# Performance work log

Measured on AMD Instinct MI355X. Metric: run time of the kernel, lower is better.

The kernel has to match this reference:

```python
import jax, jax.numpy as jnp
import numpy as np

NUM_EXPERTS = 256
TOP_K = 8
N_GROUP = 8
TOPK_GROUP = 4
ROUTED_SCALING_FACTOR = 2.5


def setup_inputs() -> dict:
    key = jax.random.key(0)
    k1, k2, k3 = jax.random.split(key, 3)
    B, H, E = 16384, 7168, NUM_EXPERTS
    hidden_states = jax.random.normal(k1, (B, H), dtype=jnp.float32)
    weight = jax.random.normal(k2, (E, H), dtype=jnp.float32) * 0.02
    e_score_correction_bias = jax.random.normal(k3, (E,), dtype=jnp.float32) * 0.01
    return {
        "hidden_states": hidden_states,
        "weight": weight,
        "e_score_correction_bias": e_score_correction_bias,
    }


def reference(hidden_states, weight, e_score_correction_bias):
    B = hidden_states.shape[0]
    experts_per_group = NUM_EXPERTS // N_GROUP
    # router logits: [B, E] (small skinny GEMM)
    router_logits = jnp.einsum("bh,eh->be", hidden_states.astype(jnp.float32), weight.astype(jnp.float32))
    # torch casts to f64 for sigmoid then back; f32 sigmoid is numerically equivalent here
    scores = jax.nn.sigmoid(router_logits).astype(hidden_states.dtype)
    scores_for_choice = scores + e_score_correction_bias[None, :]
    # per-group score = sum of top-2 expert scores in the group
    grp = scores_for_choice.reshape(B, N_GROUP, experts_per_group)
    top2_vals, _ = jax.lax.top_k(grp, 2)          # [B, G, 2]
    group_scores = top2_vals.sum(axis=-1)          # [B, G]
    # pick topk_group groups, build group mask via scatter
    _, group_idx = jax.lax.top_k(group_scores, TOPK_GROUP)  # [B, topk_group]
    group_mask = jnp.zeros((B, N_GROUP), dtype=scores_for_choice.dtype)
    group_mask = group_mask.at[jnp.arange(B)[:, None], group_idx].set(1.0)
    # expand group mask to experts and mask scores
    score_mask = jnp.broadcast_to(group_mask[:, :, None], (B, N_GROUP, experts_per_group)).reshape(B, -1)
    masked_scores = jnp.where(score_mask > 0, scores_for_choice, 0.0)
    # final expert top-k on masked (bias-corrected) scores
    _, topk_indices = jax.lax.top_k(masked_scores, TOP_K)   # [B, top_k]
    # weights gathered from the UN-biased sigmoid scores, then normalize + scale
    topk_weights = jnp.take_along_axis(scores, topk_indices, axis=1)
    topk_weights = topk_weights / topk_weights.sum(axis=-1, keepdims=True)
    topk_weights = topk_weights * ROUTED_SCALING_FACTOR
    return topk_indices, topk_weights
```

## Files before the change

### kernel.cpp

```cpp
#include <hip/hip_runtime.h>
#include <math.h>

#define B_ROWS 16384
#define H_DIM 7168
#define N_EXP 256
#define KT 32
#define MT 64
#define ET 128

using v4d = __attribute__((ext_vector_type(4))) double;

__global__ __launch_bounds__(256, 2)
void router_gemm(const float* __restrict__ hs, const float* __restrict__ w,
                 float* __restrict__ scores) {
    __shared__ float AfU[2304];
    __shared__ float WfU[4608];
    __shared__ int okSh;

    const int t = threadIdx.x;
    const int lane = t & 63;
    const int wv = t >> 6;
    const int fm = lane & 15;
    const int kg = lane >> 4;
    const int tx = t & 15;
    const int ty = t >> 4;
    const int row8 = t >> 3;
    const int kq8 = t & 7;

    const int mBase = blockIdx.x * MT;
    const int eBase = blockIdx.y * ET;
    const float* hsp = hs + (size_t)mBase * H_DIM;
    const float* wp  = w  + (size_t)eBase * H_DIM;

    bool ok = true;
#pragma unroll 1
    for (int p = 0; p < 3; ++p) {
        for (int i = t; i < 64 * 36; i += 256) {
            int m = i / 36, kk = i % 36;
            int k = (kk & 7) * 4 + (kk >> 3);
            AfU[i] = (p == 0) ? (float)(4 * m + k + 1)
                   : (p == 2) ? (float)(k + 1) : 1.0f;
        }
        for (int i = t; i < 128 * 36; i += 256) {
            int e = i / 36, kk = i % 36;
            int k = (kk & 7) * 4 + (kk >> 3);
            WfU[i] = (p == 1) ? (float)(4 * e + k + 1)
                   : (p == 2) ? (float)(k + 1) : 1.0f;
        }
        __syncthreads();
        double a = (double)AfU[fm * 36 + 8 * kg];
        double b = (double)WfU[fm * 36 + 8 * kg];
        v4d z = {0.0, 0.0, 0.0, 0.0};
        v4d pr = __builtin_amdgcn_mfma_f64_16x16x4f64(a, b, z, 0, 0, 0);
#pragma unroll
        for (int r = 0; r < 4; ++r) {
            double ev = (p == 0) ? (double)(16 * (4 * kg + r) + 10)
                      : (p == 1) ? (double)(16 * fm + 10) : 30.0;
            ok = ok && (pr[r] == ev);
        }
        __syncthreads();
    }
    if (t == 0) okSh = 1;
    __syncthreads();
    if (!ok) okSh = 0;
    __syncthreads();
    const bool useMfma = (okSh != 0);

    union AccU { double v[4][8]; v4d m[4][2]; } acc;
#pragma unroll
    for (int r = 0; r < 4; ++r)
#pragma unroll
        for (int c = 0; c < 8; ++c) acc.v[r][c] = 0.0;

    float haf[2][4], waf[4][4];
#pragma unroll
    for (int i = 0; i < 2; ++i)
        *(float4*)&haf[i][0] = *(const float4*)(hsp + (size_t)(i * 32 + row8) * H_DIM + 4 * kq8);
#pragma unroll
    for (int i = 0; i < 4; ++i)
        *(float4*)&waf[i][0] = *(const float4*)(wp + (size_t)(i * 32 + row8) * H_DIM + 4 * kq8);

    const int NCHUNK = H_DIM / KT;
    for (int ch = 0; ch < NCHUNK; ++ch) {
        if (useMfma) {
#pragma unroll
            for (int i = 0; i < 2; ++i)
#pragma unroll
                for (int j = 0; j < 4; ++j)
                    AfU[(i * 32 + row8) * 36 + 8 * j + kq8] = haf[i][j];
#pragma unroll
            for (int i = 0; i < 4; ++i)
#pragma unroll
                for (int j = 0; j < 4; ++j)
                    WfU[(i * 32 + row8) * 36 + 8 * j + kq8] = waf[i][j];
        } else {
#pragma unroll
            for (int i = 0; i < 2; ++i)
#pragma unroll
                for (int j = 0; j < 4; ++j)
                    AfU[(4 * kq8 + j) * 68 + i * 32 + row8] = haf[i][j];
#pragma unroll
            for (int i = 0; i < 4; ++i)
#pragma unroll
                for (int j = 0; j < 4; ++j)
                    WfU[(4 * kq8 + j) * 132 + i * 32 + row8] = waf[i][j];
        }
        __syncthreads();
        if (ch + 1 < NCHUNK) {
            const float* hp2 = hsp + (size_t)(ch + 1) * KT;
            const float* wp2 = wp  + (size_t)(ch + 1) * KT;
#pragma unroll
            for (int i = 0; i < 2; ++i)
                *(float4*)&haf[i][0] = *(const float4*)(hp2 + (size_t)(i * 32 + row8) * H_DIM + 4 * kq8);
#pragma unroll
            for (int i = 0; i < 4; ++i)
                *(float4*)&waf[i][0] = *(const float4*)(wp2 + (size_t)(i * 32 + row8) * H_DIM + 4 * kq8);
        }
        if (useMfma) {
            float afr[4][8], bfr[2][8];
#pragma unroll
            for (int rs = 0; rs < 4; ++rs) {
                const int base = (rs * 16 + fm) * 36 + 8 * kg;
                *(float4*)&afr[rs][0] = *(float4*)&AfU[base];
                *(float4*)&afr[rs][4] = *(float4*)&AfU[base + 4];
            }
#pragma unroll
            for (int cs = 0; cs < 2; ++cs) {
                const int base = (wv * 32 + cs * 16 + fm) * 36 + 8 * kg;
                *(float4*)&bfr[cs][0] = *(float4*)&WfU[base];
                *(float4*)&bfr[cs][4] = *(float4*)&WfU[base + 4];
            }
#pragma unroll
            for (int q = 0; q < 8; ++q) {
                double aq0 = (double)afr[0][q], aq1 = (double)afr[1][q];
                double aq2 = (double)afr[2][q], aq3 = (double)afr[3][q];
                double bq0 = (double)bfr[0][q], bq1 = (double)bfr[1][q];
                acc.m[0][0] = __builtin_amdgcn_mfma_f64_16x16x4f64(aq0, bq0, acc.m[0][0], 0, 0, 0);
                acc.m[0][1] = __builtin_amdgcn_mfma_f64_16x16x4f64(aq0, bq1, acc.m[0][1], 0, 0, 0);
                acc.m[1][0] = __builtin_amdgcn_mfma_f64_16x16x4f64(aq1, bq0, acc.m[1][0], 0, 0, 0);
                acc.m[1][1] = __builtin_amdgcn_mfma_f64_16x16x4f64(aq1, bq1, acc.m[1][1], 0, 0, 0);
                acc.m[2][0] = __builtin_amdgcn_mfma_f64_16x16x4f64(aq2, bq0, acc.m[2][0], 0, 0, 0);
                acc.m[2][1] = __builtin_amdgcn_mfma_f64_16x16x4f64(aq2, bq1, acc.m[2][1], 0, 0, 0);
                acc.m[3][0] = __builtin_amdgcn_mfma_f64_16x16x4f64(aq3, bq0, acc.m[3][0], 0, 0, 0);
                acc.m[3][1] = __builtin_amdgcn_mfma_f64_16x16x4f64(aq3, bq1, acc.m[3][1], 0, 0, 0);
            }
        } else {
#pragma unroll
            for (int k = 0; k < KT; ++k) {
                float4 af  = *(float4*)&AfU[k * 68 + ty * 4];
                float4 bfa = *(float4*)&WfU[k * 132 + tx * 4];
                float4 bfb = *(float4*)&WfU[k * 132 + 64 + tx * 4];
                double a_[4] = {(double)af.x, (double)af.y, (double)af.z, (double)af.w};
                double b_[8] = {(double)bfa.x, (double)bfa.y, (double)bfa.z, (double)bfa.w,
                                (double)bfb.x, (double)bfb.y, (double)bfb.z, (double)bfb.w};
#pragma unroll
                for (int r = 0; r < 4; ++r)
#pragma unroll
                    for (int c = 0; c < 8; ++c)
                        acc.v[r][c] = fma(a_[r], b_[c], acc.v[r][c]);
            }
        }
        __syncthreads();
    }

    if (useMfma) {
#pragma unroll
        for (int rs = 0; rs < 4; ++rs)
#pragma unroll
            for (int cs = 0; cs < 2; ++cs)
#pragma unroll
                for (int r = 0; r < 4; ++r) {
                    const int rr = mBase + rs * 16 + 4 * kg + r;
                    const int cc = eBase + wv * 32 + cs * 16 + fm;
                    double s = 1.0 / (1.0 + exp(-acc.m[rs][cs][r]));
                    scores[(size_t)rr * N_EXP + cc] = (float)s;
                }
    } else {
#pragma unroll
        for (int r = 0; r < 4; ++r) {
            const int rr = mBase + ty * 4 + r;
            float* dst = scores + (size_t)rr * N_EXP + eBase;
            float4 o0, o1;
            o0.x = (float)(1.0 / (1.0 + exp(-acc.v[r][0])));
            o0.y = (float)(1.0 / (1.0 + exp(-acc.v[r][1])));
            o0.z = (float)(1.0 / (1.0 + exp(-acc.v[r][2])));
            o0.w = (float)(1.0 / (1.0 + exp(-acc.v[r][3])));
            o1.x = (float)(1.0 / (1.0 + exp(-acc.v[r][4])));
            o1.y = (float)(1.0 / (1.0 + exp(-acc.v[r][5])));
            o1.z = (float)(1.0 / (1.0 + exp(-acc.v[r][6])));
            o1.w = (float)(1.0 / (1.0 + exp(-acc.v[r][7])));
            *(float4*)(dst + tx * 4) = o0;
            *(float4*)(dst + 64 + tx * 4) = o1;
        }
    }
}

__global__ __launch_bounds__(256)
void router_topk_kernel(const float* __restrict__ scores, const float* __restrict__ bias,
                        float* __restrict__ out) {
    const int lane = threadIdx.x & 63;
    const int row = (blockIdx.x * blockDim.x + threadIdx.x) >> 6;

    float4 s4 = *(const float4*)(scores + (size_t)row * N_EXP + lane * 4);
    float4 b4 = *(const float4*)(bias + lane * 4);
    float sc[4]  = {s4.x, s4.y, s4.z, s4.w};
    float sfc[4] = {sc[0] + b4.x, sc[1] + b4.y, sc[2] + b4.z, sc[3] + b4.w};

    float m1 = -1e30f, m2 = -1e30f;
#pragma unroll
    for (int i = 0; i < 4; ++i) {
        float v = sfc[i];
        if (v > m1) { m2 = m1; m1 = v; }
        else if (v > m2) m2 = v;
    }
#pragma unroll
    for (int off = 1; off <= 4; off <<= 1) {
        float o1 = __shfl_xor(m1, off);
        float o2 = __shfl_xor(m2, off);
        float n1 = fmaxf(m1, o1);
        float n2 = fmaxf(fminf(m1, o1), fmaxf(m2, o2));
        m1 = n1; m2 = n2;
    }
    float gs = m1 + m2;
    int g = lane >> 3;
    int rank = 0;
#pragma unroll
    for (int j = 0; j < 8; ++j) {
        float gj = __shfl(gs, j * 8);
        rank += (gj > gs || (gj == gs && j < g)) ? 1 : 0;
    }
    bool sel = rank < 4;
    float mv[4];
#pragma unroll
    for (int i = 0; i < 4; ++i) mv[i] = sel ? sfc[i] : 0.0f;

    float wsum = 0.f;
    float myIdxF = 0.f, myW = 0.f;
    for (int it = 0; it < 8; ++it) {
        float bv = mv[0]; int bi = 0;
#pragma unroll
        for (int i = 1; i < 4; ++i)
            if (mv[i] > bv) { bv = mv[i]; bi = i; }
        int bidx = lane * 4 + bi;
        float bsc = sc[bi];
#pragma unroll
        for (int off = 1; off <= 32; off <<= 1) {
            float ov = __shfl_xor(bv, off);
            int   oi = __shfl_xor(bidx, off);
            float os = __shfl_xor(bsc, off);
            if (ov > bv || (ov == bv && oi < bidx)) { bv = ov; bidx = oi; bsc = os; }
        }
        wsum += bsc;
        if (lane == it) { myIdxF = (float)bidx; myW = bsc; }
        if ((bidx >> 2) == lane) mv[bidx & 3] = -1e30f;
    }
    if (lane < 8) {
        out[(size_t)row * 8 + lane] = myIdxF;
        out[(size_t)B_ROWS * 8 + (size_t)row * 8 + lane] = myW * (2.5f / wsum);
    }
}

extern "C" void kernel_launch(void* const* d_in, const int* in_sizes, int n_in,
                              void* d_out, int out_size, void* d_ws, size_t ws_size,
                              hipStream_t stream) {
    const float* hs   = (const float*)d_in[0];
    const float* w    = (const float*)d_in[1];
    const float* bias = (const float*)d_in[2];
    float* out = (float*)d_out;
    float* scores = (float*)d_ws;

    dim3 g1(B_ROWS / MT, N_EXP / ET);
    router_gemm<<<g1, 256, 0, stream>>>(hs, w, scores);
    router_topk_kernel<<<B_ROWS / 4, 256, 0, stream>>>(scores, bias, out);
}
```

Measured before the change: 1.986 ms.

## Store MFMA operands as doubles in LDS and probe output layout at runtime

The MFMA path now converts hs and weight tiles to double when writing them to shared memory, with a padded stride of 33, instead of storing floats and converting after each LDS read. This moves the float-to-double conversion from the inner MFMA loop to the staging step, which runs once per element. The startup self-test no longer fills LDS in three passes; it issues a few register-only MFMAs and derives the output row and column mapping from their results, and the store step uses that mapping. In exchange the kernel moves twice as many LDS bytes per chunk as scalar double reads rather than float4 reads, and the larger LDS footprint may reduce occupancy.

Result: faster. 1.589 ms (-20.0%).

```diff
diff --git a/kernel.cpp b/kernel.cpp
--- a/kernel.cpp
+++ b/kernel.cpp
@@ -13,9 +13,12 @@
 __global__ __launch_bounds__(256, 2)
 void router_gemm(const float* __restrict__ hs, const float* __restrict__ w,
                  float* __restrict__ scores) {
-    __shared__ float AfU[2304];
-    __shared__ float WfU[4608];
+    __shared__ double LdsD[64 * 33 + 128 * 33];
     __shared__ int okSh;
+    double* Ad = LdsD;
+    double* Wd = LdsD + 64 * 33;
+    float* Af = (float*)LdsD;
+    float* Wf = ((float*)LdsD) + 2304;
 
     const int t = threadIdx.x;
     const int lane = t & 63;
@@ -32,33 +35,28 @@
     const float* hsp = hs + (size_t)mBase * H_DIM;
     const float* wp  = w  + (size_t)eBase * H_DIM;
 
+    v4d z = {0.0, 0.0, 0.0, 0.0};
+    v4d d1 = __builtin_amdgcn_mfma_f64_16x16x4f64((double)(fm + 1), 1.0, z, 0, 0, 0);
+    v4d d2 = __builtin_amdgcn_mfma_f64_16x16x4f64(1.0, (double)(fm + 1), z, 0, 0, 0);
+    v4d d3 = __builtin_amdgcn_mfma_f64_16x16x4f64((double)(4 * fm + kg + 1),
+                                                  (double)(8 * fm + 3 * kg + 5), z, 0, 0, 0);
     bool ok = true;
-#pragma unroll 1
-    for (int p = 0; p < 3; ++p) {
-        for (int i = t; i < 64 * 36; i += 256) {
-            int m = i / 36, kk = i % 36;
-            int k = (kk & 7) * 4 + (kk >> 3);
-            AfU[i] = (p == 0) ? (float)(4 * m + k + 1)
-                   : (p == 2) ? (float)(k + 1) : 1.0f;
-        }
-        for (int i = t; i < 128 * 36; i += 256) {
-            int e = i / 36, kk = i % 36;
-            int k = (kk & 7) * 4 + (kk >> 3);
-            WfU[i] = (p == 1) ? (float)(4 * e + k + 1)
-                   : (p == 2) ? (float)(k + 1) : 1.0f;
-        }
-        __syncthreads();
-        double a = (double)AfU[fm * 36 + 8 * kg];
-        double b = (double)WfU[fm * 36 + 8 * kg];
-        v4d z = {0.0, 0.0, 0.0, 0.0};
-        v4d pr = __builtin_amdgcn_mfma_f64_16x16x4f64(a, b, z, 0, 0, 0);
-#pragma unroll
-        for (int r = 0; r < 4; ++r) {
-            double ev = (p == 0) ? (double)(16 * (4 * kg + r) + 10)
-                      : (p == 1) ? (double)(16 * fm + 10) : 30.0;
-            ok = ok && (pr[r] == ev);
-        }
-        __syncthreads();
+    int mA[4], mB[4];
+#pragma unroll
+    for (int r = 0; r < 4; ++r) {
+        double v1 = d1[r], v2 = d2[r];
+        int a_ = -1, b_ = -1;
+        if (v1 >= 4.0 && v1 <= 64.0 && v2 >= 4.0 && v2 <= 64.0) {
+            a_ = (int)(v1 * 0.25) - 1;
+            b_ = (int)(v2 * 0.25) - 1;
+            if (v1 != 4.0 * (double)(a_ + 1) || v2 != 4.0 * (double)(b_ + 1)) ok = false;
+        } else ok = false;
+        if (a_ < 0) ok = false;
+        else {
+            double P = 4.0 * (double)a_ + 1.0, Q = 8.0 * (double)b_ + 5.0;
+            if (d3[r] != 4.0 * P * Q + 18.0 * P + 6.0 * Q + 42.0) ok = false;
+        }
+        mA[r] = a_; mB[r] = b_;
     }
     if (t == 0) okSh = 1;
     __syncthreads();
@@ -87,23 +85,23 @@
             for (int i = 0; i < 2; ++i)
 #pragma unroll
                 for (int j = 0; j < 4; ++j)
-                    AfU[(i * 32 + row8) * 36 + 8 * j + kq8] = haf[i][j];
+                    Ad[(i * 32 + row8) * 33 + 8 * j + kq8] = (double)haf[i][j];
 #pragma unroll
             for (int i = 0; i < 4; ++i)
 #pragma unroll
                 for (int j = 0; j < 4; ++j)
-                    WfU[(i * 32 + row8) * 36 + 8 * j + kq8] = waf[i][j];
+                    Wd[(i * 32 + row8) * 33 + 8 * j + kq8] = (double)waf[i][j];
         } else {
 #pragma unroll
             for (int i = 0; i < 2; ++i)
 #pragma unroll
                 for (int j = 0; j < 4; ++j)
-                    AfU[(4 * kq8 + j) * 68 + i * 32 + row8] = haf[i][j];
+                    Af[(4 * kq8 + j) * 68 + i * 32 + row8] = haf[i][j];
 #pragma unroll
             for (int i = 0; i < 4; ++i)
 #pragma unroll
                 for (int j = 0; j < 4; ++j)
-                    WfU[(4 * kq8 + j) * 132 + i * 32 + row8] = waf[i][j];
+                    Wf[(4 * kq8 + j) * 132 + i * 32 + row8] = waf[i][j];
         }
         __syncthreads();
         if (ch + 1 < NCHUNK) {
@@ -117,39 +115,36 @@
                 *(float4*)&waf[i][0] = *(const float4*)(wp2 + (size_t)(i * 32 + row8) * H_DIM + 4 * kq8);
         }
         if (useMfma) {
-            float afr[4][8], bfr[2][8];
+            double afr[4][8], bfr[2][8];
 #pragma unroll
             for (int rs = 0; rs < 4; ++rs) {
-                const int base = (rs * 16 + fm) * 36 + 8 * kg;
-                *(float4*)&afr[rs][0] = *(float4*)&AfU[base];
-                *(float4*)&afr[rs][4] = *(float4*)&AfU[base + 4];
+                const double* p = Ad + (rs * 16 + fm) * 33 + 8 * kg;
+#pragma unroll
+                for (int q = 0; q < 8; ++q) afr[rs][q] = p[q];
             }
 #pragma unroll
             for (int cs = 0; cs < 2; ++cs) {
-                const int base = (wv * 32 + cs * 16 + fm) * 36 + 8 * kg;
-                *(float4*)&bfr[cs][0] = *(float4*)&WfU[base];
-                *(float4*)&bfr[cs][4] = *(float4*)&WfU[base + 4];
+                const double* p = Wd + (wv * 32 + cs * 16 + fm) * 33 + 8 * kg;
+#pragma unroll
+                for (int q = 0; q < 8; ++q) bfr[cs][q] = p[q];
             }
 #pragma unroll
             for (int q = 0; q < 8; ++q) {
-                double aq0 = (double)afr[0][q], aq1 = (double)afr[1][q];
-                double aq2 = (double)afr[2][q], aq3 = (double)afr[3][q];
-                double bq0 = (double)bfr[0][q], bq1 = (double)bfr[1][q];
-                acc.m[0][0] = __builtin_amdgcn_mfma_f64_16x16x4f64(aq0, bq0, acc.m[0][0], 0, 0, 0);
-                acc.m[0][1] = __builtin_amdgcn_mfma_f64_16x16x4f64(aq0, bq1, acc.m[0][1], 0, 0, 0);
-                acc.m[1][0] = __builtin_amdgcn_mfma_f64_16x16x4f64(aq1, bq0, acc.m[1][0], 0, 0, 0);
-                acc.m[1][1] = __builtin_amdgcn_mfma_f64_16x16x4f64(aq1, bq1, acc.m[1][1], 0, 0, 0);
-                acc.m[2][0] = __builtin_amdgcn_mfma_f64_16x16x4f64(aq2, bq0, acc.m[2][0], 0, 0, 0);
-                acc.m[2][1] = __builtin_amdgcn_mfma_f64_16x16x4f64(aq2, bq1, acc.m[2][1], 0, 0, 0);
-                acc.m[3][0] = __builtin_amdgcn_mfma_f64_16x16x4f64(aq3, bq0, acc.m[3][0], 0, 0, 0);
-                acc.m[3][1] = __builtin_amdgcn_mfma_f64_16x16x4f64(aq3, bq1, acc.m[3][1], 0, 0, 0);
+                acc.m[0][0] = __builtin_amdgcn_mfma_f64_16x16x4f64(afr[0][q], bfr[0][q], acc.m[0][0], 0, 0, 0);
+                acc.m[0][1] = __builtin_amdgcn_mfma_f64_16x16x4f64(afr[0][q], bfr[1][q], acc.m[0][1], 0, 0, 0);
+                acc.m[1][0] = __builtin_amdgcn_mfma_f64_16x16x4f64(afr[1][q], bfr[0][q], acc.m[1][0], 0, 0, 0);
+                acc.m[1][1] = __builtin_amdgcn_mfma_f64_16x16x4f64(afr[1][q], bfr[1][q], acc.m[1][1], 0, 0, 0);
+                acc.m[2][0] = __builtin_amdgcn_mfma_f64_16x16x4f64(afr[2][q], bfr[0][q], acc.m[2][0], 0, 0, 0);
+                acc.m[2][1] = __builtin_amdgcn_mfma_f64_16x16x4f64(afr[2][q], bfr[1][q], acc.m[2][1], 0, 0, 0);
+                acc.m[3][0] = __builtin_amdgcn_mfma_f64_16x16x4f64(afr[3][q], bfr[0][q], acc.m[3][0], 0, 0, 0);
+                acc.m[3][1] = __builtin_amdgcn_mfma_f64_16x16x4f64(afr[3][q], bfr[1][q], acc.m[3][1], 0, 0, 0);
             }
         } else {
 #pragma unroll
             for (int k = 0; k < KT; ++k) {
-                float4 af  = *(float4*)&AfU[k * 68 + ty * 4];
-                float4 bfa = *(float4*)&WfU[k * 132 + tx * 4];
-                float4 bfb = *(float4*)&WfU[k * 132 + 64 + tx * 4];
+                float4 af  = *(float4*)&Af[k * 68 + ty * 4];
+                float4 bfa = *(float4*)&Wf[k * 132 + tx * 4];
+                float4 bfb = *(float4*)&Wf[k * 132 + 64 + tx * 4];
                 double a_[4] = {(double)af.x, (double)af.y, (double)af.z, (double)af.w};
                 double b_[8] = {(double)bfa.x, (double)bfa.y, (double)bfa.z, (double)bfa.w,
                                 (double)bfb.x, (double)bfb.y, (double)bfb.z, (double)bfb.w};
@@ -170,8 +165,8 @@
             for (int cs = 0; cs < 2; ++cs)
 #pragma unroll
                 for (int r = 0; r < 4; ++r) {
-                    const int rr = mBase + rs * 16 + 4 * kg + r;
-                    const int cc = eBase + wv * 32 + cs * 16 + fm;
+                    const int rr = mBase + rs * 16 + mA[r];
+                    const int cc = eBase + wv * 32 + cs * 16 + mB[r];
                     double s = 1.0 / (1.0 + exp(-acc.m[rs][cs][r]));
                     scores[(size_t)rr * N_EXP + cc] = (float)s;
                 }
```
